# Performance work log

Hardware: AMD Instinct MI355X
Metric: run time of the kernel (lower is better)

## Reference

```python
import jax, jax.numpy as jnp
import numpy as np

DIM = 1024
NUM_HEADS = 16
HEAD_DIM = DIM // NUM_HEADS
SCALE = HEAD_DIM ** (-0.5)


def setup_inputs() -> dict:
    key = jax.random.key(0)
    k_x, k_qkv, k_ow, k_ob = jax.random.split(key, 4)
    x = jax.random.normal(k_x, (4, 2048, DIM), dtype=jnp.float32)
    # nn.Linear(dim, 3*dim, bias=False): store as [dim, 3*dim] for x @ W
    w_qkv = jax.random.normal(k_qkv, (DIM, 3 * DIM), dtype=jnp.float32) * (DIM ** -0.5)
    w_out = jax.random.normal(k_ow, (DIM, DIM), dtype=jnp.float32) * (DIM ** -0.5)
    b_out = jax.random.normal(k_ob, (DIM,), dtype=jnp.float32) * 0.02
    return {"x": x, "w_qkv": w_qkv, "w_out": w_out, "b_out": b_out}


def reference(x, w_qkv, w_out, b_out):
    B, S, D = x.shape
    H, Hd = NUM_HEADS, HEAD_DIM
    qkv = x @ w_qkv                                  # [B, S, 3*D]
    # rearrange 'b s (v h d) -> v b h s d'
    qkv = qkv.reshape(B, S, 3, H, Hd).transpose(2, 0, 3, 1, 4)
    q, k, v = qkv[0], qkv[1], qkv[2]                 # each [B, H, S, Hd]
    scores = jnp.einsum('bhqd,bhkd->bhqk', q, k) * SCALE
    attn = jax.nn.softmax(scores, axis=-1)
    out = jnp.einsum('bhqk,bhkd->bhqd', attn, v)     # [B, H, S, Hd]
    out = out.transpose(0, 2, 1, 3).reshape(B, S, D)  # 'b h s d -> b s (h d)'
    return out @ w_out + b_out
```

## Files before the change

### kernel.cpp

```cpp
#include <hip/hip_runtime.h>
#include <hip/hip_bf16.h>
#include <stdint.h>

typedef __bf16 bf16_t;
typedef __bf16 bf16x4 __attribute__((ext_vector_type(4)));
typedef __bf16 bf16x8 __attribute__((ext_vector_type(8)));
typedef float f32x4 __attribute__((ext_vector_type(4)));
typedef unsigned short u16;

#define L2E 1.4426950408889634f
#define MC 69.249473f

__device__ __forceinline__ void async_load16(const bf16_t* g, bf16_t* l) {
  __builtin_amdgcn_global_load_lds(
      (__attribute__((address_space(1))) uint32_t*)g,
      (__attribute__((address_space(3))) uint32_t*)l, 16, 0, 0);
}

__global__ void detect_k(const uint16_t* __restrict__ x, int* __restrict__ flag) {
  if (blockIdx.x != 0) return;
  const int lane = threadIdx.x & 63;
  int bad = 0;
#pragma unroll
  for (int p = 0; p < 4; ++p) {
    const int i = lane * 4 + p;
    uint16_t h = x[2 * i];
    int e = (h >> 7) & 0xFF;
    if (e == 0 || e >= 0xBD) bad++;
  }
  bad += __shfl_xor(bad, 1, 64);
  bad += __shfl_xor(bad, 2, 64);
  bad += __shfl_xor(bad, 4, 64);
  bad += __shfl_xor(bad, 8, 64);
  bad += __shfl_xor(bad, 16, 64);
  bad += __shfl_xor(bad, 32, 64);
  if (lane == 0 && threadIdx.x < 64) *flag = (bad > 32) ? 1 : 0;
}

__global__ void convert_k(const void* __restrict__ in, bf16_t* __restrict__ out,
                          int n, const int* __restrict__ flag) {
  const int f = *flag;
  const int i0 = blockIdx.x * blockDim.x + threadIdx.x;
  const int stride = gridDim.x * blockDim.x;
  if (f) {
    const float* p = (const float*)in;
    for (int i = i0; i < n; i += stride) {
      float v = p[i];
      v = (v == v) ? v : 0.f;
      v = fminf(fmaxf(v, -1e6f), 1e6f);
      out[i] = (bf16_t)v;
    }
  } else {
    const bf16_t* p = (const bf16_t*)in;
    for (int i = i0; i < n; i += stride) {
      float v = (float)p[i];
      v = (v == v) ? v : 0.f;
      v = fminf(fmaxf(v, -1e6f), 1e6f);
      out[i] = (bf16_t)v;
    }
  }
}

__global__ __launch_bounds__(256) void wtrans_k(const void* __restrict__ in,
                                                bf16_t* __restrict__ out, int R,
                                                int C, const int* __restrict__ flag) {
  __shared__ u16 tile[64][65];
  const int f = *flag;
  const int tr = blockIdx.y * 64, tc = blockIdx.x * 64;
  const int t = threadIdx.x;
#pragma unroll
  for (int i = 0; i < 16; ++i) {
    int idx = i * 256 + t, r = idx >> 6, c = idx & 63;
    float v;
    if (f)
      v = ((const float*)in)[(size_t)(tr + r) * C + tc + c];
    else
      v = (float)((const bf16_t*)in)[(size_t)(tr + r) * C + tc + c];
    v = (v == v) ? v : 0.f;
    v = fminf(fmaxf(v, -1e6f), 1e6f);
    bf16_t b = (bf16_t)v;
    tile[r][c] = *(u16*)&b;
  }
  __syncthreads();
#pragma unroll
  for (int i = 0; i < 16; ++i) {
    int idx = i * 256 + t, r = idx >> 6, c = idx & 63;
    ((u16*)out)[(size_t)(tc + r) * R + tr + c] = tile[c][r];
  }
}

__device__ __forceinline__ void gemm_bt_mainloop(
    const bf16_t* __restrict__ A, const bf16_t* __restrict__ Bt, int K, int m0,
    int n0, bf16_t* As, bf16_t* Bs, f32x4 acc[4][4]) {
  const int t = threadIdx.x, lane = t & 63, w = t >> 6;
  const int l15 = lane & 15, quad = lane >> 4;
  const int wm = (w >> 1) * 64, wn = (w & 1) * 64;
  const int srow = w * 16 + (lane >> 2);
  const int sk = (lane & 3) * 8;
  const bf16_t* gA = A + (size_t)(m0 + srow) * K + sk;
  const bf16_t* gB = Bt + (size_t)(n0 + srow) * K + sk;
  bf16_t* lA = As + w * 512;
  bf16_t* lB = Bs + w * 512;
  const size_t gstep = (size_t)64 * K;

  for (int kt = 0; kt < K; kt += 32) {
    __syncthreads();
    async_load16(gA, lA);
    async_load16(gA + gstep, lA + 2048);
    async_load16(gB, lB);
    async_load16(gB + gstep, lB + 2048);
    gA += 32;
    gB += 32;
    __syncthreads();
    bf16x8 af[4], bfr[4];
#pragma unroll
    for (int f = 0; f < 4; ++f) {
      af[f] = *(const bf16x8*)(As + (wm + f * 16 + l15) * 32 + quad * 8);
      bfr[f] = *(const bf16x8*)(Bs + (wn + f * 16 + l15) * 32 + quad * 8);
    }
#pragma unroll
    for (int i = 0; i < 4; ++i)
#pragma unroll
      for (int j = 0; j < 4; ++j)
        acc[i][j] =
            __builtin_amdgcn_mfma_f32_16x16x32_bf16(af[i], bfr[j], acc[i][j], 0, 0, 0);
  }
}

__global__ __launch_bounds__(256) void qkv_gemm_k(const bf16_t* __restrict__ X,
                                                  const bf16_t* __restrict__ WqT,
                                                  bf16_t* __restrict__ qo,
                                                  bf16_t* __restrict__ ko,
                                                  bf16_t* __restrict__ vto) {
  __shared__ __align__(16) bf16_t As[128 * 32];
  __shared__ __align__(16) bf16_t Bs[128 * 32];
  const int m0 = blockIdx.y * 128, n0 = blockIdx.x * 128;
  f32x4 acc[4][4];
  const f32x4 z = {0.f, 0.f, 0.f, 0.f};
#pragma unroll
  for (int i = 0; i < 4; ++i)
#pragma unroll
    for (int j = 0; j < 4; ++j) acc[i][j] = z;
  gemm_bt_mainloop(X, WqT, 1024, m0, n0, As, Bs, acc);

  const int lane = threadIdx.x & 63, w = threadIdx.x >> 6;
  const int l15 = lane & 15, quad = lane >> 4;
  const int wm = (w >> 1) * 64, wn = (w & 1) * 64;
#pragma unroll
  for (int j = 0; j < 4; ++j) {
    const int gnb = n0 + wn + j * 16;
    const int vi = gnb >> 10;
    const int rem = gnb & 1023;
    const int h = rem >> 6;
    const int d = (rem & 63) + l15;
    if (vi == 2) {
#pragma unroll
      for (int i = 0; i < 4; ++i) {
        const int gm0 = m0 + wm + i * 16 + quad * 4;
        const int b = gm0 >> 11, s = gm0 & 2047;
        bf16x4 pv;
#pragma unroll
        for (int r = 0; r < 4; ++r) pv[r] = (bf16_t)acc[i][j][r];
        *(bf16x4*)(vto + ((size_t)(b * 16 + h) * 64 + d) * 2048 + s) = pv;
      }
    } else {
      const float scale = (vi == 0) ? 0.125f : 1.0f;
      bf16_t* dst = (vi == 0) ? qo : ko;
#pragma unroll
      for (int i = 0; i < 4; ++i) {
#pragma unroll
        for (int r = 0; r < 4; ++r) {
          const int gm = m0 + wm + i * 16 + quad * 4 + r;
          const int b = gm >> 11, s = gm & 2047;
          dst[(((size_t)(b * 16 + h) * 2048 + s) << 6) + d] =
              (bf16_t)(acc[i][j][r] * scale);
        }
      }
    }
  }
}

__global__ __launch_bounds__(256) void out_gemm_k(const bf16_t* __restrict__ Ain,
                                                  const bf16_t* __restrict__ WoT,
                                                  const bf16_t* __restrict__ bias,
                                                  void* __restrict__ outp,
                                                  const int* __restrict__ flag) {
  __shared__ __align__(16) bf16_t As[128 * 32];
  __shared__ __align__(16) bf16_t Bs[128 * 32];
  const int m0 = blockIdx.y * 128, n0 = blockIdx.x * 128;
  f32x4 acc[4][4];
  const f32x4 z = {0.f, 0.f, 0.f, 0.f};
#pragma unroll
  for (int i = 0; i < 4; ++i)
#pragma unroll
    for (int j = 0; j < 4; ++j) acc[i][j] = z;
  gemm_bt_mainloop(Ain, WoT, 1024, m0, n0, As, Bs, acc);

  const int f32out = *flag;
  const int lane = threadIdx.x & 63, w = threadIdx.x >> 6;
  const int l15 = lane & 15, quad = lane >> 4;
  const int wm = (w >> 1) * 64, wn = (w & 1) * 64;
#pragma unroll
  for (int j = 0; j < 4; ++j) {
    const int gn = n0 + wn + j * 16 + l15;
    const float bv = (float)bias[gn];
#pragma unroll
    for (int i = 0; i < 4; ++i) {
#pragma unroll
      for (int r = 0; r < 4; ++r) {
        const int gm = m0 + wm + i * 16 + quad * 4 + r;
        const float val = acc[i][j][r] + bv;
        if (f32out)
          ((float*)outp)[(size_t)gm * 1024 + gn] = val;
        else
          ((bf16_t*)outp)[(size_t)gm * 1024 + gn] = (bf16_t)val;
      }
    }
  }
}

#define KTILE 4096

__global__ __launch_bounds__(256, 2) void attn_k(const bf16_t* __restrict__ q,
                                                 const bf16_t* __restrict__ k,
                                                 const bf16_t* __restrict__ vt,
                                                 bf16_t* __restrict__ o) {
  __shared__ __align__(16) bf16_t Ps[256 * 64];
  __shared__ __align__(16) bf16_t Ks[2 * KTILE];
  __shared__ __align__(16) bf16_t Vts[2 * KTILE];

  const int t = threadIdx.x, lane = t & 63, w = t >> 6;
  const int l15 = lane & 15, quad = lane >> 4;
  const int x = blockIdx.x;
  const int j = x >> 3;
  const int bh = (x & 7) * 8 + (j >> 3);
  const int qt = j & 7;
  const bf16_t* qp = q + ((size_t)bh * 2048 + qt * 256) * 64;
  const bf16_t* kp = k + (size_t)bh * 2048 * 64;
  const bf16_t* vp = vt + (size_t)bh * 64 * 2048;

  const int lane8 = lane >> 3, lc = lane & 7;
  int kOff[2], vOff[2], ldsOff[2];
#pragma unroll
  for (int c = 0; c < 2; ++c) {
    const int rho = (w * 2 + c) * 8 + lane8;
    const int srow = (rho >> 4) + (rho & 15) * 4;
    const int col = (lc ^ (rho & 7)) * 8;
    kOff[c] = srow * 64 + col;
    vOff[c] = rho * 2048 + col;
    ldsOff[c] = (w * 2 + c) * 512;
  }

#pragma unroll
  for (int c = 0; c < 2; ++c) {
    async_load16(kp + kOff[c], Ks + ldsOff[c]);
    async_load16(vp + vOff[c], Vts + ldsOff[c]);
  }
#pragma unroll
  for (int p = 0; p < 8; ++p) {
    const int off = p * 2048 + t * 8;
    async_load16(qp + off, Ps + off);
  }
  __syncthreads();

  bf16x8 qf[4][2];
#pragma unroll
  for (int qs = 0; qs < 4; ++qs)
#pragma unroll
    for (int ks = 0; ks < 2; ++ks)
      qf[qs][ks] = *(const bf16x8*)(Ps + (w * 64 + qs * 16 + l15) * 64 +
                                    ks * 32 + quad * 8);

  f32x4 acc[4][4];
  const f32x4 z = {0.f, 0.f, 0.f, 0.f};
  float lsum[4][4];
#pragma unroll
  for (int qs = 0; qs < 4; ++qs)
#pragma unroll
    for (int f = 0; f < 4; ++f) {
      acc[qs][f] = z;
      lsum[qs][f] = 0.f;
    }

  bf16_t* psw = Ps + w * 64 * 64;

  for (int kt = 0; kt < 32; ++kt) {
    const int b = kt & 1;
    if (kt < 31) {
      const int bn = b ^ 1;
#pragma unroll
      for (int c = 0; c < 2; ++c) {
        async_load16(kp + (size_t)(kt + 1) * KTILE + kOff[c],
                     Ks + bn * KTILE + ldsOff[c]);
        async_load16(vp + (size_t)(kt + 1) * 64 + vOff[c],
                     Vts + bn * KTILE + ldsOff[c]);
      }
    }

    const bf16_t* Kb = Ks + b * KTILE;
    const bf16_t* Vb = Vts + b * KTILE;

    f32x4 sacc[4][4];
#pragma unroll
    for (int qs = 0; qs < 4; ++qs)
#pragma unroll
      for (int f = 0; f < 4; ++f) sacc[qs][f] = z;
#pragma unroll
    for (int ks = 0; ks < 2; ++ks) {
      const int cx = (((ks * 4 + quad) ^ (l15 & 7)) * 8);
      bf16x8 kf[4];
#pragma unroll
      for (int f = 0; f < 4; ++f)
        kf[f] = *(const bf16x8*)(Kb + (f * 16 + l15) * 64 + cx);
      __builtin_amdgcn_s_setprio(1);
#pragma unroll
      for (int qs = 0; qs < 4; ++qs)
#pragma unroll
        for (int f = 0; f < 4; ++f)
          sacc[qs][f] = __builtin_amdgcn_mfma_f32_16x16x32_bf16(
              qf[qs][ks], kf[f], sacc[qs][f], 0, 0, 0);
      __builtin_amdgcn_s_setprio(0);
    }

#pragma unroll
    for (int qs = 0; qs < 4; ++qs)
#pragma unroll
      for (int r = 0; r < 4; ++r) {
        bf16x4 pk;
        float ls = 0.f;
#pragma unroll
        for (int f = 0; f < 4; ++f) {
          const float pv = __builtin_amdgcn_exp2f(
              fminf(fmaf(sacc[qs][f][r], L2E, -MC), 0.f));
          ls += pv;
          pk[f] = (bf16_t)pv;
        }
        lsum[qs][r] += ls;
        const int row = qs * 16 + quad * 4 + r;
        *(bf16x4*)(psw + row * 64 + ((l15 >> 1) ^ (row & 7)) * 8 +
                   (l15 & 1) * 4) = pk;
      }

#pragma unroll
    for (int ks = 0; ks < 2; ++ks) {
      const int cx = (((ks * 4 + quad) ^ (l15 & 7)) * 8);
      bf16x8 vf[4];
#pragma unroll
      for (int f = 0; f < 4; ++f)
        vf[f] = *(const bf16x8*)(Vb + (f * 16 + l15) * 64 + cx);
#pragma unroll
      for (int qs = 0; qs < 4; ++qs) {
        bf16x8 pf = *(const bf16x8*)(psw + (qs * 16 + l15) * 64 +
                                     ((ks * 4 + quad) ^ (l15 & 7)) * 8);
        __builtin_amdgcn_s_setprio(1);
#pragma unroll
        for (int f = 0; f < 4; ++f)
          acc[qs][f] = __builtin_amdgcn_mfma_f32_16x16x32_bf16(
              pf, vf[f], acc[qs][f], 0, 0, 0);
        __builtin_amdgcn_s_setprio(0);
      }
    }

    if (kt < 31) __syncthreads();
  }

#pragma unroll
  for (int qs = 0; qs < 4; ++qs)
#pragma unroll
    for (int r = 0; r < 4; ++r) {
      float s = lsum[qs][r];
      s += __shfl_xor(s, 1, 64);
      s += __shfl_xor(s, 2, 64);
      s += __shfl_xor(s, 4, 64);
      s += __shfl_xor(s, 8, 64);
      lsum[qs][r] = 1.0f / fmaxf(s, 1e-37f);
    }

  const int b = bh >> 4, h = bh & 15;
#pragma unroll
  for (int qs = 0; qs < 4; ++qs)
#pragma unroll
    for (int r = 0; r < 4; ++r) {
      const int srow = qt * 256 + w * 64 + qs * 16 + quad * 4 + r;
      const float inv = lsum[qs][r];
#pragma unroll
      for (int f = 0; f < 4; ++f) {
        const int d = f * 16 + l15;
        o[(size_t)(b * 2048 + srow) * 1024 + h * 64 + d] =
            (bf16_t)(acc[qs][f][r] * inv);
      }
    }
}

extern "C" void kernel_launch(void* const* d_in, const int* in_sizes, int n_in,
                              void* d_out, int out_size, void* d_ws, size_t ws_size,
                              hipStream_t stream) {
  const void* x_raw = d_in[0];
  const void* wqkv_raw = d_in[1];
  const void* wout_raw = d_in[2];
  const void* bout_raw = d_in[3];

  const int nx = 4 * 2048 * 1024;
  const int nwq = 1024 * 3072;
  const int nwo = 1024 * 1024;
  const int nb = 1024;

  char* ws = (char*)d_ws;
  int* flag = (int*)ws;
  bf16_t* xb = (bf16_t*)(ws + 256);
  bf16_t* wqbT = xb + nx;
  bf16_t* wobT = wqbT + nwq;
  bf16_t* bob = wobT + nwo;
  bf16_t* qb = bob + nb;
  const size_t bhsd = (size_t)4 * 16 * 2048 * 64;
  bf16_t* kb = qb + bhsd;
  bf16_t* vtb = kb + bhsd;
  bf16_t* ab = xb;

  detect_k<<<1, 64, 0, stream>>>((const uint16_t*)x_raw, flag);
  convert_k<<<2048, 256, 0, stream>>>(x_raw, xb, nx, flag);
  wtrans_k<<<dim3(3072 / 64, 1024 / 64), 256, 0, stream>>>(wqkv_raw, wqbT, 1024,
                                                           3072, flag);
  wtrans_k<<<dim3(1024 / 64, 1024 / 64), 256, 0, stream>>>(wout_raw, wobT, 1024,
                                                           1024, flag);
  convert_k<<<4, 256, 0, stream>>>(bout_raw, bob, nb, flag);

  qkv_gemm_k<<<dim3(3072 / 128, 8192 / 128), 256, 0, stream>>>(xb, wqbT, qb, kb,
                                                               vtb);
  attn_k<<<dim3(512), 256, 0, stream>>>(qb, kb, vtb, ab);
  out_gemm_k<<<dim3(1024 / 128, 8192 / 128), 256, 0, stream>>>(ab, wobT, bob,
                                                               d_out, flag);
}
```

Baseline: 300.4 us.

## Fold softmax scale into Q, seed scores with offset, compute row sums via MFMA

Q is pre-scaled by scale*log2(e) in the QKV epilogue, and the score MFMA starts from a constant -MC accumulator, so the per-element fma before exp2 disappears. Row sums of P are now taken with an extra MFMA against a ones vector instead of scalar adds and a cross-lane shuffle reduction. This trades VALU work for one extra MFMA per P fragment. Sums now come from bf16-rounded probabilities, which slightly changes numerics.

```diff
diff --git a/kernel.cpp b/kernel.cpp
--- a/kernel.cpp
+++ b/kernel.cpp
@@ -10,6 +10,7 @@
 
 #define L2E 1.4426950408889634f
 #define MC 69.249473f
+#define QSC 0.18033688f
 
 __device__ __forceinline__ void async_load16(const bf16_t* g, bf16_t* l) {
   __builtin_amdgcn_global_load_lds(
@@ -164,7 +165,7 @@
         *(bf16x4*)(vto + ((size_t)(b * 16 + h) * 64 + d) * 2048 + s) = pv;
       }
     } else {
-      const float scale = (vi == 0) ? 0.125f : 1.0f;
+      const float scale = (vi == 0) ? QSC : 1.0f;
       bf16_t* dst = (vi == 0) ? qo : ko;
 #pragma unroll
       for (int i = 0; i < 4; ++i) {
@@ -271,16 +272,18 @@
       qf[qs][ks] = *(const bf16x8*)(Ps + (w * 64 + qs * 16 + l15) * 64 +
                                     ks * 32 + quad * 8);
 
-  f32x4 acc[4][4];
+  f32x4 acc[4][4], asum[4];
   const f32x4 z = {0.f, 0.f, 0.f, 0.f};
-  float lsum[4][4];
-#pragma unroll
-  for (int qs = 0; qs < 4; ++qs)
-#pragma unroll
-    for (int f = 0; f < 4; ++f) {
-      acc[qs][f] = z;
-      lsum[qs][f] = 0.f;
-    }
+  const f32x4 minit = {-MC, -MC, -MC, -MC};
+  bf16x8 onesf;
+#pragma unroll
+  for (int i = 0; i < 8; ++i) onesf[i] = (bf16_t)1.0f;
+#pragma unroll
+  for (int qs = 0; qs < 4; ++qs) {
+    asum[qs] = z;
+#pragma unroll
+    for (int f = 0; f < 4; ++f) acc[qs][f] = z;
+  }
 
   bf16_t* psw = Ps + w * 64 * 64;
 
@@ -301,13 +304,8 @@
     const bf16_t* Vb = Vts + b * KTILE;
 
     f32x4 sacc[4][4];
-#pragma unroll
-    for (int qs = 0; qs < 4; ++qs)
-#pragma unroll
-      for (int f = 0; f < 4; ++f) sacc[qs][f] = z;
-#pragma unroll
-    for (int ks = 0; ks < 2; ++ks) {
-      const int cx = (((ks * 4 + quad) ^ (l15 & 7)) * 8);
+    {
+      const int cx = ((quad ^ (l15 & 7)) * 8);
       bf16x8 kf[4];
 #pragma unroll
       for (int f = 0; f < 4; ++f)
@@ -318,7 +316,22 @@
 #pragma unroll
         for (int f = 0; f < 4; ++f)
           sacc[qs][f] = __builtin_amdgcn_mfma_f32_16x16x32_bf16(
-              qf[qs][ks], kf[f], sacc[qs][f], 0, 0, 0);
+              qf[qs][0], kf[f], minit, 0, 0, 0);
+      __builtin_amdgcn_s_setprio(0);
+    }
+    {
+      const int cx = (((4 + quad) ^ (l15 & 7)) * 8);
+      bf16x8 kf[4];
+#pragma unroll
+      for (int f = 0; f < 4; ++f)
+        kf[f] = *(const bf16x8*)(Kb + (f * 16 + l15) * 64 + cx);
+      __builtin_amdgcn_s_setprio(1);
+#pragma unroll
+      for (int qs = 0; qs < 4; ++qs)
+#pragma unroll
+        for (int f = 0; f < 4; ++f)
+          sacc[qs][f] = __builtin_amdgcn_mfma_f32_16x16x32_bf16(
+              qf[qs][1], kf[f], sacc[qs][f], 0, 0, 0);
       __builtin_amdgcn_s_setprio(0);
     }
 
@@ -327,15 +340,10 @@
 #pragma unroll
       for (int r = 0; r < 4; ++r) {
         bf16x4 pk;
-        float ls = 0.f;
-#pragma unroll
-        for (int f = 0; f < 4; ++f) {
-          const float pv = __builtin_amdgcn_exp2f(
-              fminf(fmaf(sacc[qs][f][r], L2E, -MC), 0.f));
-          ls += pv;
-          pk[f] = (bf16_t)pv;
-        }
-        lsum[qs][r] += ls;
+#pragma unroll
+        for (int f = 0; f < 4; ++f)
+          pk[f] =
+              (bf16_t)__builtin_amdgcn_exp2f(fminf(sacc[qs][f][r], 0.f));
         const int row = qs * 16 + quad * 4 + r;
         *(bf16x4*)(psw + row * 64 + ((l15 >> 1) ^ (row & 7)) * 8 +
                    (l15 & 1) * 4) = pk;
@@ -357,24 +365,14 @@
         for (int f = 0; f < 4; ++f)
           acc[qs][f] = __builtin_amdgcn_mfma_f32_16x16x32_bf16(
               pf, vf[f], acc[qs][f], 0, 0, 0);
+        asum[qs] = __builtin_amdgcn_mfma_f32_16x16x32_bf16(pf, onesf, asum[qs],
+                                                           0, 0, 0);
         __builtin_amdgcn_s_setprio(0);
       }
     }
 
     if (kt < 31) __syncthreads();
   }
-
-#pragma unroll
-  for (int qs = 0; qs < 4; ++qs)
-#pragma unroll
-    for (int r = 0; r < 4; ++r) {
-      float s = lsum[qs][r];
-      s += __shfl_xor(s, 1, 64);
-      s += __shfl_xor(s, 2, 64);
-      s += __shfl_xor(s, 4, 64);
-      s += __shfl_xor(s, 8, 64);
-      lsum[qs][r] = 1.0f / fmaxf(s, 1e-37f);
-    }
 
   const int b = bh >> 4, h = bh & 15;
 #pragma unroll
@@ -382,7 +380,7 @@
 #pragma unroll
     for (int r = 0; r < 4; ++r) {
       const int srow = qt * 256 + w * 64 + qs * 16 + quad * 4 + r;
-      const float inv = lsum[qs][r];
+      const float inv = 1.0f / fmaxf(asum[qs][r], 1e-37f);
 #pragma unroll
       for (int f = 0; f < 4; ++f) {
         const int d = f * 16 + l15;
```

New measurement: 291.6 us. 1.03x faster.
